# Kernel tuning notes

Measured on AMD Instinct MI355X. Metric: run time of the kernel, lower is better.

## Reference

```python
import jax, jax.numpy as jnp
import numpy as np

N, E, D = 50000, 200000, 128   # graph nodes, graph edges (= line-graph nodes), feature dim
L = 2                          # number of GINEConv iterations (linegraph init arg)


def _build_line_graph(col0, col1):
    """Exact sparse equivalent of torch.nonzero((col1[:,None]==col0[None,:]) & (col0[:,None]!=col1[:,None])).
    Returns line edges (i -> j) with col1[i] == col0[j] and edge i not a self-loop,
    plus edge_attr_idx = col1[lg_src] (the shared graph node)."""
    order = np.argsort(col0, kind='stable')              # edges grouped by source node
    counts = np.bincount(col0, minlength=N)              # out-degree per node
    offsets = np.concatenate([[0], np.cumsum(counts)[:-1]])
    lengths = np.where(col0 != col1, counts[col1], 0)    # successors of each non-self-loop edge
    M = int(lengths.sum())
    lg_src = np.repeat(np.arange(E), lengths)
    cum = np.cumsum(lengths)
    pos = np.arange(M) - np.repeat(cum - lengths, lengths)  # position within each successor block
    lg_dst = order[np.repeat(offsets[col1], lengths) + pos]
    edge_attr_idx = col1[lg_src]
    return lg_src.astype(np.int64), lg_dst.astype(np.int64), edge_attr_idx.astype(np.int64)


def setup_inputs() -> dict:
    rng = np.random.RandomState(0)
    col0 = rng.randint(0, N, size=E).astype(np.int64)
    col1 = rng.randint(0, N, size=E).astype(np.int64)
    lg_src, lg_dst, edge_attr_idx = _build_line_graph(col0, col1)

    key = jax.random.key(0)
    kx, k1, k2 = jax.random.split(key, 3)
    scale = (2.0 / D) ** 0.5
    return {
        'x':  jax.random.normal(kx, (N, D), dtype=jnp.float32),
        'W1': jax.random.normal(k1, (D, D), dtype=jnp.float32) * scale,
        'b1': jnp.zeros((D,), dtype=jnp.float32),
        'W2': jax.random.normal(k2, (D, D), dtype=jnp.float32) * scale,
        'b2': jnp.zeros((D,), dtype=jnp.float32),
        'col0': jnp.asarray(col0),
        'col1': jnp.asarray(col1),
        'lg_src': jnp.asarray(lg_src),
        'lg_dst': jnp.asarray(lg_dst),
        'edge_attr_idx': jnp.asarray(edge_attr_idx),
    }


def reference(x, W1, b1, W2, b2, col0, col1, lg_src, lg_dst, edge_attr_idx):
    # line-graph node features: mean of endpoint features of each original edge
    lgX = 0.5 * (x[col0] + x[col1])                       # [E, D]
    lgE = x[edge_attr_idx]                                # [M, D] line-edge attrs (fixed across iterations)

    for _ in range(L):  # GINEConv, eps = 0 (PyG default)
        m = jax.nn.relu(lgX[lg_src] + lgE)                # [M, D] messages
        aggr = jax.ops.segment_sum(m, lg_dst, num_segments=E)  # scatter-add at target line-nodes
        h = lgX + aggr                                    # (1 + eps) * x + aggr
        lgX = jax.nn.relu(h @ W1 + b1) @ W2 + b2          # gin_nn MLP

    # scatter_mean back to graph nodes by col1 (zeros where no incident edge, matching pad)
    sums = jax.ops.segment_sum(lgX, col1, num_segments=N)                     # [N, D]
    cnt = jax.ops.segment_sum(jnp.ones((lgX.shape[0], 1), lgX.dtype), col1, num_segments=N)
    gx = jnp.where(cnt > 0, sums / jnp.maximum(cnt, 1.0), 0.0)

    out = jax.nn.relu(gx)
    # dropout p=0.0 -> identity; residual=True
    return x + out
```

## Files before the change

### kernel.cpp

```cpp
#include <hip/hip_runtime.h>
#include <hip/hip_bf16.h>

constexpr int NN = 50000;
constexpr int EE = 200000;
typedef __bf16 bf16x8 __attribute__((ext_vector_type(8)));
typedef float f32x4 __attribute__((ext_vector_type(4)));

__device__ __forceinline__ float b2f(unsigned short s) {
    union { unsigned u; float f; } c; c.u = ((unsigned)s) << 16; return c.f;
}
__device__ __forceinline__ unsigned short f2b(float f) {
    union { float f; unsigned u; } c; c.f = f;
    unsigned u = c.u + 0x7fffu + ((c.u >> 16) & 1u);
    return (unsigned short)(u >> 16);
}
__device__ __forceinline__ float xv(const void* p, long i, int f32m) {
    return f32m ? ((const float*)p)[i] : b2f(((const unsigned short*)p)[i]);
}
__device__ __forceinline__ int iv(const int* p, int i, int i64m) {
    return i64m ? p[2 * i] : p[i];
}

__global__ void k_detect(const unsigned short* x16, const int* c32, int* flg) {
    __shared__ int sf, si;
    int t = threadIdx.x;
    if (t == 0) { sf = 0; si = 1; }
    __syncthreads();
    for (int i = t; i < 16384; i += 256)
        if (((x16[i] >> 7) & 0xFF) == 0xFF) sf = 1;
    if (t < 64)
        if (c32[2 * t + 1] != 0) si = 0;
    __syncthreads();
    if (t == 0) { flg[0] = sf; flg[1] = si; }
}

__global__ void k_zero(unsigned* p, int n) {
    int i = blockIdx.x * 256 + threadIdx.x;
    if (i < n) p[i] = 0u;
}

__global__ void k_wfrag(const void* W, unsigned short* Wf, const int* flg) {
    int f32m = flg[0];
    int chunk = blockIdx.x * 256 + threadIdx.x;
    if (chunk >= 2048) return;
    int l = chunk & 63, c = (chunk >> 6) & 3, t = chunk >> 8;
    int n = t * 16 + (l & 15), k0 = c * 32 + ((l >> 4) * 8);
    for (int j = 0; j < 8; j++) Wf[chunk * 8 + j] = f2b(xv(W, (long)(k0 + j) * 128 + n, f32m));
}

__global__ void k_hist(const int* col1, int* counts, const int* flg) {
    int e = blockIdx.x * 256 + threadIdx.x;
    if (e >= EE) return;
    atomicAdd(&counts[iv(col1, e, flg[1])], 1);
}

__global__ void k_scan1(const int* counts, int* bsum) {
    __shared__ int sh[256];
    int b = blockIdx.x, t = threadIdx.x;
    int idx = b * 256 + t;
    sh[t] = (idx < NN) ? counts[idx] : 0;
    __syncthreads();
    for (int off = 128; off > 0; off >>= 1) {
        if (t < off) sh[t] += sh[t + off];
        __syncthreads();
    }
    if (t == 0) bsum[b] = sh[0];
}

__global__ void k_scan2(const int* counts, const int* bsum,
                        int* row_ptr, int* cursor) {
    __shared__ int sh[256];
    __shared__ int base_s;
    int b = blockIdx.x, t = threadIdx.x;
    sh[t] = (t < b) ? bsum[t] : 0;
    __syncthreads();
    for (int off = 128; off > 0; off >>= 1) {
        if (t < off) sh[t] += sh[t + off];
        __syncthreads();
    }
    if (t == 0) base_s = sh[0];
    __syncthreads();
    int idx = b * 256 + t;
    int v = (idx < NN) ? counts[idx] : 0;
    sh[t] = v;
    __syncthreads();
    for (int off = 1; off < 256; off <<= 1) {
        int add = (t >= off) ? sh[t - off] : 0;
        __syncthreads();
        sh[t] += add;
        __syncthreads();
    }
    int ex = base_s + sh[t] - v;
    if (idx < NN) { row_ptr[idx] = ex; cursor[idx] = ex; }
    if (idx == NN - 1) row_ptr[NN] = ex + v;
}

__global__ void k_cscatter(const int* col0, const int* col1, int* cursor,
                           unsigned* elist, int* aux, const int* flg) {
    int e = blockIdx.x * 256 + threadIdx.x;
    if (e >= EE) return;
    int i64m = flg[1];
    int a = iv(col0, e, i64m), b = iv(col1, e, i64m);
    int pos = atomicAdd(&cursor[b], 1);
    elist[pos] = (unsigned)e | (a == b ? 0x80000000u : 0u);
    aux[pos] = a;
}

__global__ void k_gath(const void* x, const unsigned short* lgX,
                       const int* row_ptr, const unsigned* elist, const int* aux,
                       unsigned short* S, const int* flg, int mode) {
    int n = blockIdx.x * 4 + (threadIdx.x >> 6);
    if (n >= NN) return;
    int l = threadIdx.x & 63, k0 = l * 2;
    int f32m = flg[0];
    int lo = row_ptr[n], hi = row_ptr[n + 1];
    float xn0, xn1;
    if (f32m) {
        xn0 = ((const float*)x)[(size_t)n * 128 + k0];
        xn1 = ((const float*)x)[(size_t)n * 128 + k0 + 1];
    } else {
        unsigned u = *(const unsigned*)((const unsigned short*)x + (size_t)n * 128 + k0);
        xn0 = b2f((unsigned short)u); xn1 = b2f((unsigned short)(u >> 16));
    }
    float a0 = 0.0f, a1 = 0.0f;
    if (mode == 1) {
        if (f32m) {
            for (int p = lo; p < hi; p++) {
                unsigned pk = elist[p];
                if (pk & 0x80000000u) continue;
                const float* xa = (const float*)x + (size_t)aux[p] * 128 + k0;
                a0 += fmaxf(0.5f * xa[0] + 1.5f * xn0, 0.0f);
                a1 += fmaxf(0.5f * xa[1] + 1.5f * xn1, 0.0f);
            }
        } else {
            for (int p = lo; p < hi; p++) {
                unsigned pk = elist[p];
                if (pk & 0x80000000u) continue;
                unsigned u = *(const unsigned*)((const unsigned short*)x + (size_t)aux[p] * 128 + k0);
                a0 += fmaxf(0.5f * b2f((unsigned short)u) + 1.5f * xn0, 0.0f);
                a1 += fmaxf(0.5f * b2f((unsigned short)(u >> 16)) + 1.5f * xn1, 0.0f);
            }
        }
    } else {
        for (int p = lo; p < hi; p++) {
            unsigned pk = elist[p];
            if (pk & 0x80000000u) continue;
            int e = (int)(pk & 0x7fffffffu);
            unsigned u = *(const unsigned*)(lgX + (size_t)e * 128 + k0);
            a0 += fmaxf(b2f((unsigned short)u) + xn0, 0.0f);
            a1 += fmaxf(b2f((unsigned short)(u >> 16)) + xn1, 0.0f);
        }
    }
    unsigned o = ((unsigned)f2b(a1) << 16) | (unsigned)f2b(a0);
    *(unsigned*)(S + (size_t)n * 128 + k0) = o;
}

__global__ __launch_bounds__(256, 5)
void k_fused(const unsigned short* A, const unsigned short* S,
             const int* col0in, const int* col1in, const void* x,
             const unsigned short* Wf1, const unsigned short* Wf2,
             const void* bias1, const void* bias2,
             unsigned short* Out, const int* flg, int initA) {
    __shared__ unsigned short Lds[8192];
    int f32m = flg[0], i64m = flg[1];
    int tid = threadIdx.x;
    int w = tid >> 6, l = tid & 63;
    int lq = l >> 4, ln = l & 15;
    int e0 = blockIdx.x * 64 + w * 16;
    unsigned short* W_ = Lds + w * 2048;

    int row = e0 + ln;
    int aN = iv(col0in, row, i64m);
    int bN = initA ? iv(col1in, row, i64m) : 0;
    for (int c = 0; c < 4; c++) {
        int k0 = c * 32 + lq * 8;
        uint4 svv = *(const uint4*)(S + (size_t)aN * 128 + k0);
        const unsigned short* sp = (const unsigned short*)&svv;
        unsigned short v[8];
        if (initA) {
            if (f32m) {
                const float* xa = (const float*)x + (size_t)aN * 128 + k0;
                const float* xb = (const float*)x + (size_t)bN * 128 + k0;
                for (int j = 0; j < 8; j++)
                    v[j] = f2b(0.5f * (xa[j] + xb[j]) + b2f(sp[j]));
            } else {
                uint4 xav = *(const uint4*)((const unsigned short*)x + (size_t)aN * 128 + k0);
                uint4 xbv = *(const uint4*)((const unsigned short*)x + (size_t)bN * 128 + k0);
                const unsigned short* xa = (const unsigned short*)&xav;
                const unsigned short* xb = (const unsigned short*)&xbv;
                for (int j = 0; j < 8; j++)
                    v[j] = f2b(0.5f * (b2f(xa[j]) + b2f(xb[j])) + b2f(sp[j]));
            }
        } else {
            uint4 av = *(const uint4*)(A + (size_t)row * 128 + k0);
            const unsigned short* ap = (const unsigned short*)&av;
            for (int j = 0; j < 8; j++) v[j] = f2b(b2f(ap[j]) + b2f(sp[j]));
        }
        *(uint4*)(W_ + (c * 64 + l) * 8) = *(const uint4*)v;
    }

    f32x4 acc[8];
    for (int j = 0; j < 8; j++)
        for (int r = 0; r < 4; r++) acc[j][r] = 0.0f;
    for (int c = 0; c < 4; c++) {
        bf16x8 af = *(const bf16x8*)(W_ + (c * 64 + l) * 8);
        for (int j = 0; j < 8; j++) {
            bf16x8 bf = *(const bf16x8*)(Wf1 + (size_t)(((j * 4 + c) * 64 + l) * 8));
            acc[j] = __builtin_amdgcn_mfma_f32_16x16x32_bf16(af, bf, acc[j], 0, 0, 0);
        }
    }

    for (int j = 0; j < 8; j++) {
        int n = j * 16 + ln;
        float bv = xv(bias1, n, f32m);
        int c2 = n >> 5, lhi = ((n >> 3) & 3) * 16, j2 = n & 7;
        for (int rg = 0; rg < 4; rg++) {
            float h = acc[j][rg] + bv;
            if (h < 0.0f) h = 0.0f;
            W_[(c2 * 64 + lhi + lq * 4 + rg) * 8 + j2] = f2b(h);
        }
    }

    for (int j = 0; j < 8; j++)
        for (int r = 0; r < 4; r++) acc[j][r] = 0.0f;
    for (int c = 0; c < 4; c++) {
        bf16x8 af = *(const bf16x8*)(W_ + (c * 64 + l) * 8);
        for (int j = 0; j < 8; j++) {
            bf16x8 bf = *(const bf16x8*)(Wf2 + (size_t)(((j * 4 + c) * 64 + l) * 8));
            acc[j] = __builtin_amdgcn_mfma_f32_16x16x32_bf16(af, bf, acc[j], 0, 0, 0);
        }
    }

    for (int j = 0; j < 8; j++) {
        int n = j * 16 + ln;
        float bv = xv(bias2, n, f32m);
        for (int rg = 0; rg < 4; rg++)
            W_[(lq * 4 + rg) * 128 + n] = f2b(acc[j][rg] + bv);
    }
    for (int i = 0; i < 4; i++) {
        int idx = i * 64 + l;
        ((uint4*)Out)[(size_t)e0 * 16 + idx] = ((const uint4*)W_)[idx];
    }
}

__global__ void LGNNGINELayer_12463995093126_kernel(
    const void* x, const unsigned short* lgX, const int* row_ptr,
    const unsigned* elist, void* out, const int* flg) {
    int n = blockIdx.x * 4 + (threadIdx.x >> 6);
    if (n >= NN) return;
    int l = threadIdx.x & 63, k0 = l * 2;
    int f32m = flg[0];
    int lo = row_ptr[n], hi = row_ptr[n + 1];
    float a0 = 0.0f, a1 = 0.0f;
    for (int p = lo; p < hi; p++) {
        int e = (int)(elist[p] & 0x7fffffffu);
        unsigned u = *(const unsigned*)(lgX + (size_t)e * 128 + k0);
        a0 += b2f((unsigned short)u);
        a1 += b2f((unsigned short)(u >> 16));
    }
    float g0 = 0.0f, g1 = 0.0f;
    if (hi > lo) {
        float inv = 1.0f / (float)(hi - lo);
        g0 = fmaxf(a0 * inv, 0.0f);
        g1 = fmaxf(a1 * inv, 0.0f);
    }
    if (f32m) {
        ((float*)out)[(long)n * 128 + k0]     = ((const float*)x)[(long)n * 128 + k0] + g0;
        ((float*)out)[(long)n * 128 + k0 + 1] = ((const float*)x)[(long)n * 128 + k0 + 1] + g1;
    } else {
        unsigned u = *(const unsigned*)((const unsigned short*)x + (long)n * 128 + k0);
        float r0 = b2f((unsigned short)u) + g0;
        float r1 = b2f((unsigned short)(u >> 16)) + g1;
        unsigned o = ((unsigned)f2b(r1) << 16) | (unsigned)f2b(r0);
        *(unsigned*)((unsigned short*)out + (long)n * 128 + k0) = o;
    }
}

extern "C" void kernel_launch(void* const* d_in, const int* in_sizes, int n_in,
                              void* d_out, int out_size, void* d_ws, size_t ws_size,
                              hipStream_t stream) {
    (void)in_sizes; (void)n_in; (void)out_size; (void)ws_size;
    const void* x = d_in[0];
    const void* W1 = d_in[1];
    const void* b1 = d_in[2];
    const void* W2 = d_in[3];
    const void* b2 = d_in[4];
    const int* col0 = (const int*)d_in[5];
    const int* col1 = (const int*)d_in[6];

    char* p = (char*)d_ws;
    unsigned short* lgX = (unsigned short*)p; p += (size_t)EE * 128 * 2;
    unsigned short* S = (unsigned short*)p;   p += (size_t)NN * 128 * 2;
    int* row_ptr = (int*)p;                   p += (size_t)(NN + 16) * 4;
    int* cursor = (int*)p;                    p += (size_t)NN * 4;
    int* counts = (int*)p;                    p += (size_t)NN * 4;
    int* bsum = (int*)p;                      p += 256 * 4;
    int* aux = (int*)p;                       p += (size_t)EE * 4;
    unsigned* elist = (unsigned*)p;           p += (size_t)EE * 4;
    int* flg = (int*)p;                       p += 256;
    unsigned short* Wf1 = (unsigned short*)p; p += 16384 * 2;
    unsigned short* Wf2 = (unsigned short*)p;

    int gB = EE / 64;
    int eB = (EE + 255) / 256;
    int nB4 = (NN + 3) / 4;
    int sB = (NN + 255) / 256;

    k_detect<<<1, 256, 0, stream>>>((const unsigned short*)x, col0, flg);
    k_wfrag<<<8, 256, 0, stream>>>(W1, Wf1, flg);
    k_wfrag<<<8, 256, 0, stream>>>(W2, Wf2, flg);

    k_zero<<<(NN + 255) / 256, 256, 0, stream>>>((unsigned*)counts, NN);
    k_hist<<<eB, 256, 0, stream>>>(col1, counts, flg);
    k_scan1<<<sB, 256, 0, stream>>>(counts, bsum);
    k_scan2<<<sB, 256, 0, stream>>>(counts, bsum, row_ptr, cursor);
    k_cscatter<<<eB, 256, 0, stream>>>(col0, col1, cursor, elist, aux, flg);

    k_gath<<<nB4, 256, 0, stream>>>(x, lgX, row_ptr, elist, aux, S, flg, 1);
    k_fused<<<gB, 256, 0, stream>>>(lgX, S, col0, col1, x, Wf1, Wf2, b1, b2,
                                    lgX, flg, 1);
    k_gath<<<nB4, 256, 0, stream>>>(x, lgX, row_ptr, elist, aux, S, flg, 2);
    k_fused<<<gB, 256, 0, stream>>>(lgX, S, col0, col1, x, Wf1, Wf2, b1, b2,
                                    lgX, flg, 0);
    LGNNGINELayer_12463995093126_kernel<<<nB4, 256, 0, stream>>>(
        x, lgX, row_ptr, elist, d_out, flg);
}
```

Measured before the change: 392.5 us.

## Store line-graph features in col1-sorted edge order to make gathers contiguous

Line-graph node features are now stored in the CSR order produced by the counting sort on col1, rather than in original edge order. The per-node gather kernels then read consecutive rows of lgX instead of going through an indirect edge-id lookup, and the elist array is dropped. The fused MLP kernel reads endpoints from the permuted aux/node1 arrays, and its launch-bounds occupancy hint is raised. Row order inside each node segment depends on atomic ordering, so float summation order may vary between runs, and the higher occupancy target may force register spills.

New measurement: 379.7 us. 3.3% less time.

```diff
diff --git a/kernel.cpp b/kernel.cpp
--- a/kernel.cpp
+++ b/kernel.cpp
@@ -96,18 +96,18 @@
 }
 
 __global__ void k_cscatter(const int* col0, const int* col1, int* cursor,
-                           unsigned* elist, int* aux, const int* flg) {
+                           unsigned* aux, int* node1, const int* flg) {
     int e = blockIdx.x * 256 + threadIdx.x;
     if (e >= EE) return;
     int i64m = flg[1];
     int a = iv(col0, e, i64m), b = iv(col1, e, i64m);
     int pos = atomicAdd(&cursor[b], 1);
-    elist[pos] = (unsigned)e | (a == b ? 0x80000000u : 0u);
-    aux[pos] = a;
+    aux[pos] = (unsigned)a | (a == b ? 0x80000000u : 0u);
+    node1[pos] = b;
 }
 
 __global__ void k_gath(const void* x, const unsigned short* lgX,
-                       const int* row_ptr, const unsigned* elist, const int* aux,
+                       const int* row_ptr, const unsigned* aux,
                        unsigned short* S, const int* flg, int mode) {
     int n = blockIdx.x * 4 + (threadIdx.x >> 6);
     if (n >= NN) return;
@@ -126,27 +126,25 @@
     if (mode == 1) {
         if (f32m) {
             for (int p = lo; p < hi; p++) {
-                unsigned pk = elist[p];
-                if (pk & 0x80000000u) continue;
-                const float* xa = (const float*)x + (size_t)aux[p] * 128 + k0;
+                unsigned av = aux[p];
+                if (av & 0x80000000u) continue;
+                const float* xa = (const float*)x + (size_t)av * 128 + k0;
                 a0 += fmaxf(0.5f * xa[0] + 1.5f * xn0, 0.0f);
                 a1 += fmaxf(0.5f * xa[1] + 1.5f * xn1, 0.0f);
             }
         } else {
             for (int p = lo; p < hi; p++) {
-                unsigned pk = elist[p];
-                if (pk & 0x80000000u) continue;
-                unsigned u = *(const unsigned*)((const unsigned short*)x + (size_t)aux[p] * 128 + k0);
+                unsigned av = aux[p];
+                if (av & 0x80000000u) continue;
+                unsigned u = *(const unsigned*)((const unsigned short*)x + (size_t)av * 128 + k0);
                 a0 += fmaxf(0.5f * b2f((unsigned short)u) + 1.5f * xn0, 0.0f);
                 a1 += fmaxf(0.5f * b2f((unsigned short)(u >> 16)) + 1.5f * xn1, 0.0f);
             }
         }
     } else {
         for (int p = lo; p < hi; p++) {
-            unsigned pk = elist[p];
-            if (pk & 0x80000000u) continue;
-            int e = (int)(pk & 0x7fffffffu);
-            unsigned u = *(const unsigned*)(lgX + (size_t)e * 128 + k0);
+            if (aux[p] & 0x80000000u) continue;
+            unsigned u = *(const unsigned*)(lgX + (size_t)p * 128 + k0);
             a0 += fmaxf(b2f((unsigned short)u) + xn0, 0.0f);
             a1 += fmaxf(b2f((unsigned short)(u >> 16)) + xn1, 0.0f);
         }
@@ -155,14 +153,14 @@
     *(unsigned*)(S + (size_t)n * 128 + k0) = o;
 }
 
-__global__ __launch_bounds__(256, 5)
+__global__ __launch_bounds__(256, 8)
 void k_fused(const unsigned short* A, const unsigned short* S,
-             const int* col0in, const int* col1in, const void* x,
+             const unsigned* aux, const int* node1, const void* x,
              const unsigned short* Wf1, const unsigned short* Wf2,
              const void* bias1, const void* bias2,
              unsigned short* Out, const int* flg, int initA) {
     __shared__ unsigned short Lds[8192];
-    int f32m = flg[0], i64m = flg[1];
+    int f32m = flg[0];
     int tid = threadIdx.x;
     int w = tid >> 6, l = tid & 63;
     int lq = l >> 4, ln = l & 15;
@@ -170,8 +168,8 @@
     unsigned short* W_ = Lds + w * 2048;
 
     int row = e0 + ln;
-    int aN = iv(col0in, row, i64m);
-    int bN = initA ? iv(col1in, row, i64m) : 0;
+    int aN = (int)(aux[row] & 0x7fffffffu);
+    int bN = initA ? node1[row] : 0;
     for (int c = 0; c < 4; c++) {
         int k0 = c * 32 + lq * 8;
         uint4 svv = *(const uint4*)(S + (size_t)aN * 128 + k0);
@@ -245,7 +243,7 @@
 
 __global__ void LGNNGINELayer_12463995093126_kernel(
     const void* x, const unsigned short* lgX, const int* row_ptr,
-    const unsigned* elist, void* out, const int* flg) {
+    void* out, const int* flg) {
     int n = blockIdx.x * 4 + (threadIdx.x >> 6);
     if (n >= NN) return;
     int l = threadIdx.x & 63, k0 = l * 2;
@@ -253,8 +251,7 @@
     int lo = row_ptr[n], hi = row_ptr[n + 1];
     float a0 = 0.0f, a1 = 0.0f;
     for (int p = lo; p < hi; p++) {
-        int e = (int)(elist[p] & 0x7fffffffu);
-        unsigned u = *(const unsigned*)(lgX + (size_t)e * 128 + k0);
+        unsigned u = *(const unsigned*)(lgX + (size_t)p * 128 + k0);
         a0 += b2f((unsigned short)u);
         a1 += b2f((unsigned short)(u >> 16));
     }
@@ -295,8 +292,8 @@
     int* cursor = (int*)p;                    p += (size_t)NN * 4;
     int* counts = (int*)p;                    p += (size_t)NN * 4;
     int* bsum = (int*)p;                      p += 256 * 4;
-    int* aux = (int*)p;                       p += (size_t)EE * 4;
-    unsigned* elist = (unsigned*)p;           p += (size_t)EE * 4;
+    unsigned* aux = (unsigned*)p;             p += (size_t)EE * 4;
+    int* node1 = (int*)p;                     p += (size_t)EE * 4;
     int* flg = (int*)p;                       p += 256;
     unsigned short* Wf1 = (unsigned short*)p; p += 16384 * 2;
     unsigned short* Wf2 = (unsigned short*)p;
@@ -314,14 +311,14 @@
     k_hist<<<eB, 256, 0, stream>>>(col1, counts, flg);
     k_scan1<<<sB, 256, 0, stream>>>(counts, bsum);
     k_scan2<<<sB, 256, 0, stream>>>(counts, bsum, row_ptr, cursor);
-    k_cscatter<<<eB, 256, 0, stream>>>(col0, col1, cursor, elist, aux, flg);
-
-    k_gath<<<nB4, 256, 0, stream>>>(x, lgX, row_ptr, elist, aux, S, flg, 1);
-    k_fused<<<gB, 256, 0, stream>>>(lgX, S, col0, col1, x, Wf1, Wf2, b1, b2,
+    k_cscatter<<<eB, 256, 0, stream>>>(col0, col1, cursor, aux, node1, flg);
+
+    k_gath<<<nB4, 256, 0, stream>>>(x, lgX, row_ptr, aux, S, flg, 1);
+    k_fused<<<gB, 256, 0, stream>>>(lgX, S, aux, node1, x, Wf1, Wf2, b1, b2,
                                     lgX, flg, 1);
-    k_gath<<<nB4, 256, 0, stream>>>(x, lgX, row_ptr, elist, aux, S, flg, 2);
-    k_fused<<<gB, 256, 0, stream>>>(lgX, S, col0, col1, x, Wf1, Wf2, b1, b2,
+    k_gath<<<nB4, 256, 0, stream>>>(x, lgX, row_ptr, aux, S, flg, 2);
+    k_fused<<<gB, 256, 0, stream>>>(lgX, S, aux, node1, x, Wf1, Wf2, b1, b2,
                                     lgX, flg, 0);
     LGNNGINELayer_12463995093126_kernel<<<nB4, 256, 0, stream>>>(
-        x, lgX, row_ptr, elist, d_out, flg);
-}
+        x, lgX, row_ptr, d_out, flg);
+}
```
